# Optimization experiments

Hardware: AMD Instinct MI355X
Metric: run time of the kernel (lower is better)

## Reference

```python
import jax, jax.numpy as jnp
import numpy as np

W_PAD = 1  # reflection pad / stencil half-width
CLAMP_MIN = 0.071
EPS = 1e-05


def _laplacian_kernel():
    k = 2 * W_PAD + 1
    ker = -jnp.ones((1, 1, k, k, k), dtype=jnp.float32)
    ker = ker.at[0, 0, W_PAD, W_PAD, W_PAD].set(float(k * k * k - 1))
    return ker  # [O=1, I=1, 3, 3, 3]


def _boundary_weight(pred):
    # pred: [B, L, D, H, W] raw logits
    B, L, D, H, Wd = pred.shape
    ps = jax.nn.softmax(pred, axis=1).astype(jnp.float32)
    # reflect-pad spatial dims by 1, then clamp (matches torch: pad then clamp)
    p = jnp.pad(ps, ((0, 0), (0, 0), (1, 1), (1, 1), (1, 1)), mode='reflect')
    p = jnp.clip(p, CLAMP_MIN)
    # single-channel 3x3x3 stencil applied independently per (batch, label)
    x = p.reshape(B * L, 1, D + 2, H + 2, Wd + 2)
    bt = jax.lax.conv_general_dilated(
        x, _laplacian_kernel(), window_strides=(1, 1, 1), padding='VALID',
        dimension_numbers=('NCDHW', 'OIDHW', 'NCDHW'))
    bt = jnp.abs(bt).reshape(B, L, D, H, Wd)
    bt = jax.lax.stop_gradient(bt)  # torch .detach()
    return 0.5 / (bt + 0.5)


def _dice_bpm(y_pred, y_true, bpm):
    vol_axes = tuple(range(2, y_pred.ndim))  # spatial dims
    top = 2.0 * jnp.sum(y_true * y_pred * bpm, axis=vol_axes)
    bottom = jnp.clip(jnp.sum((y_true + y_pred) * bpm, axis=vol_axes), EPS)
    return -jnp.mean(top / bottom)


def setup_inputs() -> dict:
    key = jax.random.key(0)
    k1, k2 = jax.random.split(key)
    shape = (2, 8, 128, 128, 128)
    pred = jax.random.normal(k1, shape, dtype=jnp.float32)
    target = jax.random.uniform(k2, shape, dtype=jnp.float32)
    return {"pred": pred, "target": target}


def reference(pred, target):
    focal_weight = _boundary_weight(pred)
    return _dice_bpm(pred, target, focal_weight)
```

## Files before the change

kernel.cpp:

```cpp
#include <hip/hip_runtime.h>

constexpr int Dd = 128, Hh = 128, Ww = 128;
constexpr int B_ = 2, L_ = 8;
constexpr int HW = Hh * Ww;
constexpr int S_SP = Dd * HW;
constexpr float CLAMP_MIN = 0.071f;
constexpr float EPS = 1e-5f;

constexpr int DCH = 8;
constexpr int NDC = Dd / DCH;
constexpr int HT = 4;
constexpr int NHG = Hh / HT;
constexpr int NBLK = B_ * NDC * NHG;

__global__ __launch_bounds__(256, 2) void fused_kernel(
    const float* __restrict__ pred, const float* __restrict__ tgt,
    float* __restrict__ partial) {
  const int blk = blockIdx.x;
  const int dc = blk & (NDC - 1);
  const int hg = (blk >> 4) & (NHG - 1);
  const int b  = blk >> 9;
  const int tid = threadIdx.x;
  const int wl = tid & 63;
  const int hl = tid >> 6;
  const int h = hg * HT + hl;
  const int w0 = wl * 2;
  const int d0 = dc * DCH;
  const int rtop = (hg == 0) ? 1 : hg * HT - 1;
  const int rbot = (hg == NHG - 1) ? Hh - 2 : hg * HT + HT;
  const int rotT = blk & 3;
  const int rotB = (blk + 2) & 3;
  const float* Pb = pred + (size_t)b * L_ * S_SP;
  const float* Tb = tgt  + (size_t)b * L_ * S_SP;

  __shared__ float s3[HT + 2][L_][Ww];

  float ps2[L_][2], s2c[L_][2], cprev[L_][2], rawprev[L_][2];
  float top[L_], bot[L_];
#pragma unroll
  for (int l = 0; l < L_; ++l) {
    top[l] = 0.f; bot[l] = 0.f;
    ps2[l][0] = ps2[l][1] = 0.f;
    s2c[l][0] = s2c[l][1] = 0.f;
    cprev[l][0] = cprev[l][1] = 0.f;
    rawprev[l][0] = rawprev[l][1] = 0.f;
  }

  auto rowH3 = [&](const float* rp, float (*h3)[2], float (*ctr)[2], float (*raw)[2]) {
    float2 v[L_];
#pragma unroll
    for (int l = 0; l < L_; ++l) v[l] = *(const float2*)(rp + (size_t)l * S_SP);
    float p0[L_], p1[L_];
    float s0 = 0.f, s1 = 0.f;
#pragma unroll
    for (int l = 0; l < L_; ++l) {
      p0[l] = __expf(v[l].x); s0 += p0[l];
      p1[l] = __expf(v[l].y); s1 += p1[l];
    }
    const float i0 = 1.f / s0, i1 = 1.f / s1;
#pragma unroll
    for (int l = 0; l < L_; ++l) {
      p0[l] = fmaxf(p0[l] * i0, CLAMP_MIN);
      p1[l] = fmaxf(p1[l] * i1, CLAMP_MIN);
    }
#pragma unroll
    for (int l = 0; l < L_; ++l) {
      float lf = __shfl_up(p1[l], 1, 64);
      if (wl == 0) lf = p1[l];
      float rf = __shfl_down(p0[l], 1, 64);
      if (wl == 63) rf = p0[l];
      h3[l][0] = lf + p0[l] + p1[l];
      h3[l][1] = p0[l] + p1[l] + rf;
      if (ctr) {
        ctr[l][0] = p0[l]; ctr[l][1] = p1[l];
        raw[l][0] = v[l].x; raw[l][1] = v[l].y;
      }
    }
  };

  for (int k = 0; k < DCH + 2; ++k) {
    const int t = d0 - 1 + k;
    const int rt = (t < 0) ? 1 : ((t > Dd - 1) ? Dd - 2 : t);
    const float* plane = Pb + (size_t)rt * HW;

    float h3o[L_][2], ctr[L_][2], rawc[L_][2];
    rowH3(plane + (size_t)h * Ww + w0, h3o, ctr, rawc);
    float h3t[L_][2], h3b[L_][2];
    if (hl == rotT) rowH3(plane + (size_t)rtop * Ww + w0, h3t, nullptr, nullptr);
    if (hl == rotB) rowH3(plane + (size_t)rbot * Ww + w0, h3b, nullptr, nullptr);

    __syncthreads();
#pragma unroll
    for (int l = 0; l < L_; ++l)
      *(float2*)&s3[1 + hl][l][w0] = make_float2(h3o[l][0], h3o[l][1]);
    if (hl == rotT) {
#pragma unroll
      for (int l = 0; l < L_; ++l)
        *(float2*)&s3[0][l][w0] = make_float2(h3t[l][0], h3t[l][1]);
    }
    if (hl == rotB) {
#pragma unroll
      for (int l = 0; l < L_; ++l)
        *(float2*)&s3[HT + 1][l][w0] = make_float2(h3b[l][0], h3b[l][1]);
    }
    float2 tv[L_];
    if (k >= 2) {
      const size_t base = (size_t)(t - 1) * HW + (size_t)h * Ww + w0;
#pragma unroll
      for (int l = 0; l < L_; ++l)
        tv[l] = *(const float2*)(Tb + (size_t)l * S_SP + base);
    }
    __syncthreads();

    float s2n[L_][2];
#pragma unroll
    for (int l = 0; l < L_; ++l) {
      const float2 a = *(const float2*)&s3[hl][l][w0];
      const float2 bb = *(const float2*)&s3[hl + 1][l][w0];
      const float2 c = *(const float2*)&s3[hl + 2][l][w0];
      s2n[l][0] = a.x + bb.x + c.x;
      s2n[l][1] = a.y + bb.y + c.y;
    }

    if (k >= 2) {
#pragma unroll
      for (int l = 0; l < L_; ++l) {
        {
          float bt = fabsf(27.f * cprev[l][0] - (ps2[l][0] + s2n[l][0]));
          float bw = 0.5f / (bt + 0.5f);
          top[l] += tv[l].x * rawprev[l][0] * bw;
          bot[l] += (tv[l].x + rawprev[l][0]) * bw;
        }
        {
          float bt = fabsf(27.f * cprev[l][1] - (ps2[l][1] + s2n[l][1]));
          float bw = 0.5f / (bt + 0.5f);
          top[l] += tv[l].y * rawprev[l][1] * bw;
          bot[l] += (tv[l].y + rawprev[l][1]) * bw;
        }
      }
    }

#pragma unroll
    for (int l = 0; l < L_; ++l) {
      ps2[l][0] = s2c[l][0] + s2n[l][0]; ps2[l][1] = s2c[l][1] + s2n[l][1];
      s2c[l][0] = s2n[l][0];             s2c[l][1] = s2n[l][1];
      cprev[l][0] = ctr[l][0];           cprev[l][1] = ctr[l][1];
      rawprev[l][0] = rawc[l][0];        rawprev[l][1] = rawc[l][1];
    }
  }

#pragma unroll
  for (int l = 0; l < L_; ++l) {
#pragma unroll
    for (int o = 32; o > 0; o >>= 1) {
      top[l] += __shfl_down(top[l], o, 64);
      bot[l] += __shfl_down(bot[l], o, 64);
    }
  }
  __shared__ float red[HT][16];
  if (wl == 0) {
#pragma unroll
    for (int l = 0; l < L_; ++l) {
      red[hl][2 * l]     = top[l];
      red[hl][2 * l + 1] = bot[l];
    }
  }
  __syncthreads();
  if (tid < 16) {
    float s = red[0][tid] + red[1][tid] + red[2][tid] + red[3][tid];
    partial[blk * 16 + tid] = s;
  }
}

__global__ void finalize_kernel(const float* __restrict__ partial, float* __restrict__ out) {
  __shared__ float rr[16];
  const int t = threadIdx.x;
  const int p = t >> 4;
  const int k = t & 15;
  const int b = p >> 3;
  const int l = p & 7;
  float top = 0.f, bot = 0.f;
  for (int m = 0; m < 32; ++m) {
    int blk = b * (NDC * NHG) + k * 32 + m;
    top += partial[blk * 16 + 2 * l];
    bot += partial[blk * 16 + 2 * l + 1];
  }
#pragma unroll
  for (int o = 8; o > 0; o >>= 1) {
    top += __shfl_down(top, o, 16);
    bot += __shfl_down(bot, o, 16);
  }
  if (k == 0) rr[p] = 2.f * top / fmaxf(bot, EPS);
  __syncthreads();
  if (t == 0) {
    float s = 0.f;
#pragma unroll
    for (int i = 0; i < 16; ++i) s += rr[i];
    out[0] = -s / 16.f;
  }
}

extern "C" void kernel_launch(void* const* d_in, const int* in_sizes, int n_in,
                              void* d_out, int out_size, void* d_ws, size_t ws_size,
                              hipStream_t stream) {
  const float* pred = (const float*)d_in[0];
  const float* tgt  = (const float*)d_in[1];
  float* partial = (float*)d_ws;
  fused_kernel<<<NBLK, 256, 0, stream>>>(pred, tgt, partial);
  finalize_kernel<<<1, 256, 0, stream>>>(partial, (float*)d_out);
}
```

Before: 306.1 us.

## Double H-tile to eight rows per block, swizzle block order, stream target nontemporally

Each block now covers eight H rows with 512 threads, so halo rows make up a smaller share of the work and fewer redundant softmax rows are recomputed. Block IDs are remapped so that consecutive launched blocks are spread across batch and H groups, which may improve spread across L2/XCD. The rows that compute the halos now rotate per depth step to balance work across waves. Target loads use nontemporal hints to avoid polluting cache, and the reduction scratch reuses the shared tile. Occupancy and register pressure change because of the larger block and the launch bounds of 512 threads with at least 4 blocks.

```diff
diff --git a/kernel.cpp b/kernel.cpp
--- a/kernel.cpp
+++ b/kernel.cpp
@@ -9,17 +9,18 @@
 
 constexpr int DCH = 8;
 constexpr int NDC = Dd / DCH;
-constexpr int HT = 4;
+constexpr int HT = 8;
 constexpr int NHG = Hh / HT;
 constexpr int NBLK = B_ * NDC * NHG;
 
-__global__ __launch_bounds__(256, 2) void fused_kernel(
+__global__ __launch_bounds__(512, 4) void fused_kernel(
     const float* __restrict__ pred, const float* __restrict__ tgt,
     float* __restrict__ partial) {
-  const int blk = blockIdx.x;
-  const int dc = blk & (NDC - 1);
-  const int hg = (blk >> 4) & (NHG - 1);
-  const int b  = blk >> 9;
+  const int bid = blockIdx.x;
+  const int blk = (bid & 7) * 64 + (bid >> 3);
+  const int dc = blk & 15;
+  const int hg = (blk >> 4) & 15;
+  const int b  = blk >> 8;
   const int tid = threadIdx.x;
   const int wl = tid & 63;
   const int hl = tid >> 6;
@@ -28,8 +29,6 @@
   const int d0 = dc * DCH;
   const int rtop = (hg == 0) ? 1 : hg * HT - 1;
   const int rbot = (hg == NHG - 1) ? Hh - 2 : hg * HT + HT;
-  const int rotT = blk & 3;
-  const int rotB = (blk + 2) & 3;
   const float* Pb = pred + (size_t)b * L_ * S_SP;
   const float* Tb = tgt  + (size_t)b * L_ * S_SP;
 
@@ -82,6 +81,8 @@
     const int t = d0 - 1 + k;
     const int rt = (t < 0) ? 1 : ((t > Dd - 1) ? Dd - 2 : t);
     const float* plane = Pb + (size_t)rt * HW;
+    const int rotT = (blk + k) & 7;
+    const int rotB = (blk + k + 4) & 7;
 
     float h3o[L_][2], ctr[L_][2], rawc[L_][2];
     rowH3(plane + (size_t)h * Ww + w0, h3o, ctr, rawc);
@@ -107,8 +108,11 @@
     if (k >= 2) {
       const size_t base = (size_t)(t - 1) * HW + (size_t)h * Ww + w0;
 #pragma unroll
-      for (int l = 0; l < L_; ++l)
-        tv[l] = *(const float2*)(Tb + (size_t)l * S_SP + base);
+      for (int l = 0; l < L_; ++l) {
+        unsigned long long u = __builtin_nontemporal_load(
+            (const unsigned long long*)(Tb + (size_t)l * S_SP + base));
+        tv[l] = *(float2*)&u;
+      }
     }
     __syncthreads();
 
@@ -116,10 +120,10 @@
 #pragma unroll
     for (int l = 0; l < L_; ++l) {
       const float2 a = *(const float2*)&s3[hl][l][w0];
-      const float2 bb = *(const float2*)&s3[hl + 1][l][w0];
+      const float2 m = *(const float2*)&s3[hl + 1][l][w0];
       const float2 c = *(const float2*)&s3[hl + 2][l][w0];
-      s2n[l][0] = a.x + bb.x + c.x;
-      s2n[l][1] = a.y + bb.y + c.y;
+      s2n[l][0] = a.x + m.x + c.x;
+      s2n[l][1] = a.y + m.y + c.y;
     }
 
     if (k >= 2) {
@@ -157,17 +161,20 @@
       bot[l] += __shfl_down(bot[l], o, 64);
     }
   }
-  __shared__ float red[HT][16];
+  __syncthreads();
+  float* red = (float*)s3;
   if (wl == 0) {
 #pragma unroll
     for (int l = 0; l < L_; ++l) {
-      red[hl][2 * l]     = top[l];
-      red[hl][2 * l + 1] = bot[l];
+      red[hl * 16 + 2 * l]     = top[l];
+      red[hl * 16 + 2 * l + 1] = bot[l];
     }
   }
   __syncthreads();
   if (tid < 16) {
-    float s = red[0][tid] + red[1][tid] + red[2][tid] + red[3][tid];
+    float s = 0.f;
+#pragma unroll
+    for (int w = 0; w < 8; ++w) s += red[w * 16 + tid];
     partial[blk * 16 + tid] = s;
   }
 }
@@ -180,8 +187,8 @@
   const int b = p >> 3;
   const int l = p & 7;
   float top = 0.f, bot = 0.f;
-  for (int m = 0; m < 32; ++m) {
-    int blk = b * (NDC * NHG) + k * 32 + m;
+  for (int m = 0; m < 16; ++m) {
+    int blk = b * 256 + k * 16 + m;
     top += partial[blk * 16 + 2 * l];
     bot += partial[blk * 16 + 2 * l + 1];
   }
@@ -206,6 +213,6 @@
   const float* pred = (const float*)d_in[0];
   const float* tgt  = (const float*)d_in[1];
   float* partial = (float*)d_ws;
-  fused_kernel<<<NBLK, 256, 0, stream>>>(pred, tgt, partial);
+  fused_kernel<<<NBLK, 512, 0, stream>>>(pred, tgt, partial);
   finalize_kernel<<<1, 256, 0, stream>>>(partial, (float*)d_out);
 }
```

Result: slower. 463.1 us (+51.3%).
